# Kernel optimization log

Hardware: AMD Instinct MI355X
Metric: run time of the kernel (lower is better)

Reference implementation:

```python
import jax, jax.numpy as jnp
import numpy as np

B, S, D = 1, 2048, 4096
H = 32
Q_RANK, KV_RANK = 1536, 512
NOPE, ROPE, VD = 128, 64, 128
QD = NOPE + ROPE  # 192
EPS = 1e-6
THETA = 10000.0


def setup_inputs() -> dict:
    key = jax.random.key(0)
    ks = jax.random.split(key, 8)
    std = 0.02
    return {
        'hidden_states': jax.random.normal(ks[0], (B, S, D), jnp.float32),
        'Wq_a': jax.random.normal(ks[1], (D, Q_RANK), jnp.float32) * std,
        'q_a_ln_w': jnp.ones((Q_RANK,), jnp.float32),
        'Wq_b': jax.random.normal(ks[2], (Q_RANK, H * QD), jnp.float32) * std,
        'Wkv_a': jax.random.normal(ks[3], (D, KV_RANK + ROPE), jnp.float32) * std,
        'kv_a_ln_w': jnp.ones((KV_RANK,), jnp.float32),
        'Wkv_b': jax.random.normal(ks[4], (KV_RANK, H * (NOPE + VD)), jnp.float32) * std,
        'Wo': jax.random.normal(ks[5], (H * VD, D), jnp.float32) * std,
    }


def _rmsnorm(x, w):
    return x * jax.lax.rsqrt(jnp.mean(x * x, axis=-1, keepdims=True) + EPS) * w


def _rotate_half(x):
    h = x.shape[-1] // 2
    return jnp.concatenate([-x[..., h:], x[..., :h]], axis=-1)


def _apply_rope(x, cos, sin):
    # DeepSeek interleave permutation: view(..., d//2, 2).transpose -> [evens | odds]
    xp = jnp.concatenate([x[..., 0::2], x[..., 1::2]], axis=-1)
    return xp * cos + _rotate_half(xp) * sin


def _mla_forward(hidden_states, Wq_a, q_a_ln_w, Wq_b, Wkv_a, kv_a_ln_w, Wkv_b, Wo):
    b, s, _ = hidden_states.shape
    # low-rank query projection
    q = _rmsnorm(hidden_states @ Wq_a, q_a_ln_w) @ Wq_b          # [b,s,H*QD]
    q = q.reshape(b, s, H, QD).transpose(0, 2, 1, 3)             # [b,H,s,QD]
    q_nope, q_pe = q[..., :NOPE], q[..., NOPE:]
    # compressed kv + shared rope key
    ckv = hidden_states @ Wkv_a                                   # [b,s,KV_RANK+ROPE]
    compressed, k_pe = ckv[..., :KV_RANK], ckv[..., KV_RANK:]
    kv = _rmsnorm(compressed, kv_a_ln_w) @ Wkv_b                 # [b,s,H*(NOPE+VD)]
    kv = kv.reshape(b, s, H, NOPE + VD).transpose(0, 2, 1, 3)    # [b,H,s,NOPE+VD]
    k_nope, v = kv[..., :NOPE], kv[..., NOPE:]
    k_pe = k_pe[:, None, :, :]                                    # [b,1,s,ROPE]
    # rotary tables (cos/sin duplicated halves)
    inv_freq = 1.0 / (THETA ** (jnp.arange(0, ROPE, 2, dtype=jnp.float32) / ROPE))
    freqs = jnp.outer(jnp.arange(s, dtype=jnp.float32), inv_freq)  # [s,ROPE/2]
    emb = jnp.concatenate([freqs, freqs], axis=-1)                 # [s,ROPE]
    cos = jnp.cos(emb)[None, None].astype(hidden_states.dtype)
    sin = jnp.sin(emb)[None, None].astype(hidden_states.dtype)
    q_pe = _apply_rope(q_pe, cos, sin)
    k_pe = _apply_rope(k_pe, cos, sin)
    # assemble full q/k heads
    qf = jnp.concatenate([q_nope, q_pe], axis=-1)                 # [b,H,s,QD]
    kf = jnp.concatenate([k_nope, jnp.broadcast_to(k_pe, (b, H, s, ROPE))], axis=-1)
    scale = QD ** (-0.5)
    scores = jnp.einsum('bhqd,bhkd->bhqk', qf, kf) * scale        # [b,H,s,s]
    causal = jnp.tril(jnp.ones((s, s), dtype=bool))
    scores = jnp.where(causal, scores, jnp.finfo(scores.dtype).min)
    probs = jax.nn.softmax(scores, axis=-1)
    o = jnp.einsum('bhqk,bhkd->bhqd', probs, v)                   # [b,H,s,VD]
    o = o.transpose(0, 2, 1, 3).reshape(b, s, H * VD)
    return o @ Wo


def reference(hidden_states, Wq_a, q_a_ln_w, Wq_b, Wkv_a, kv_a_ln_w, Wkv_b, Wo):
    return _mla_forward(hidden_states, Wq_a, q_a_ln_w, Wq_b, Wkv_a, kv_a_ln_w, Wkv_b, Wo)
```

## Files before the change

kernel.cpp:

```cpp
#include <hip/hip_runtime.h>

typedef unsigned short u16;
using bf16x8 = __attribute__((ext_vector_type(8))) __bf16;
using f32x4  = __attribute__((ext_vector_type(4))) float;
using s16x8  = __attribute__((ext_vector_type(8))) short;
using s16x4  = __attribute__((ext_vector_type(4))) short;

#define AS1 __attribute__((address_space(1)))
#define AS3 __attribute__((address_space(3)))

__device__ __forceinline__ void gload16(const u16* g, u16* l) {
  __builtin_amdgcn_global_load_lds((AS1 void*)(size_t)g, (AS3 void*)l, 16, 0, 0);
}

__device__ __forceinline__ u16 f2bf(float f) {
  unsigned u = __float_as_uint(f);
  u += 0x7fffu + ((u >> 16) & 1u);
  return (u16)(u >> 16);
}
__device__ __forceinline__ float bf2f(u16 h) {
  return __uint_as_float(((unsigned)h) << 16);
}

__device__ __forceinline__ void transpose_tile(const float* __restrict__ W,
                                               u16* __restrict__ WT,
                                               int K, int N, int nb, int kb,
                                               u16 (*tile)[72]) {
  const int t = threadIdx.x;
  const int rr = t >> 3;
  const int cc = (t & 7) * 8;
#pragma unroll
  for (int pass = 0; pass < 2; ++pass) {
    const float* src = W + (size_t)(kb + pass * 32 + rr) * N + nb + cc;
    float4 a = *reinterpret_cast<const float4*>(src);
    float4 b = *reinterpret_cast<const float4*>(src + 4);
    u16* tr = &tile[pass * 32 + rr][cc];
    tr[0] = f2bf(a.x); tr[1] = f2bf(a.y); tr[2] = f2bf(a.z); tr[3] = f2bf(a.w);
    tr[4] = f2bf(b.x); tr[5] = f2bf(b.y); tr[6] = f2bf(b.z); tr[7] = f2bf(b.w);
  }
  __syncthreads();
#pragma unroll
  for (int pass = 0; pass < 2; ++pass) {
    s16x8 v;
#pragma unroll
    for (int j = 0; j < 8; ++j) v[j] = (short)tile[cc + j][pass * 32 + rr];
    *reinterpret_cast<s16x8*>(WT + (size_t)(nb + pass * 32 + rr) * K + kb + cc) = v;
  }
}

__global__ __launch_bounds__(256) void prep_merged_kernel(
    const float* __restrict__ hs, u16* __restrict__ hs_bf,
    const float* __restrict__ Wqa, const float* __restrict__ Wkva, u16* __restrict__ WabT,
    const float* __restrict__ Wqb, u16* __restrict__ WqbT,
    const float* __restrict__ Wkvb, u16* __restrict__ WkvbT,
    const float* __restrict__ Wo, u16* __restrict__ WoT,
    float* __restrict__ cost, float* __restrict__ sint) {
  __shared__ u16 tile[64][72];
  const int bid = blockIdx.x, t = threadIdx.x;
  if (bid < 8192) {
    int i = (bid * 256 + t) * 4;
    float4 v = *reinterpret_cast<const float4*>(hs + i);
    s16x4 o;
    o[0] = (short)f2bf(v.x); o[1] = (short)f2bf(v.y);
    o[2] = (short)f2bf(v.z); o[3] = (short)f2bf(v.w);
    *reinterpret_cast<s16x4*>(hs_bf + i) = o;
  } else if (bid < 9728) {
    int r = bid - 8192;
    transpose_tile(Wqa, WabT, 4096, 1536, (r % 24) * 64, (r / 24) * 64, tile);
  } else if (bid < 10304) {
    int r = bid - 9728;
    transpose_tile(Wkva, WabT + (size_t)1536 * 4096, 4096, 576, (r % 9) * 64, (r / 9) * 64, tile);
  } else if (bid < 12608) {
    int r = bid - 10304;
    transpose_tile(Wqb, WqbT, 1536, 6144, (r % 96) * 64, (r / 96) * 64, tile);
  } else if (bid < 13632) {
    int r = bid - 12608;
    transpose_tile(Wkvb, WkvbT, 512, 8192, (r % 128) * 64, (r / 128) * 64, tile);
  } else if (bid < 17728) {
    int r = bid - 13632;
    transpose_tile(Wo, WoT, 4096, 4096, (r % 64) * 64, (r / 64) * 64, tile);
  } else {
    int idx = (bid - 17728) * 256 + t;
    int pos = idx >> 5, j = idx & 31;
    float inv = __expf(-(float)j * (9.210340371976184f / 32.0f));
    float f = (float)pos * inv;
    cost[idx] = cosf(f);
    sint[idx] = sinf(f);
  }
}

__global__ __launch_bounds__(256) void norms_merged_kernel(const u16* __restrict__ fused,
                                                           const float* __restrict__ qln,
                                                           const float* __restrict__ kvln,
                                                           u16* __restrict__ qan,
                                                           u16* __restrict__ cn) {
  const int bid = blockIdx.x, t = threadIdx.x;
  const int row = bid & 2047;
  const bool is_q = bid < 2048;
  const int R = is_q ? 1536 : 512;
  const u16* xr = fused + (size_t)row * 2112 + (is_q ? 0 : 1536);
  const float* w = is_q ? qln : kvln;
  u16* yr = (is_q ? qan + (size_t)row * 1536 : cn + (size_t)row * 512);
  float ss = 0.f;
  for (int i = t; i < R; i += 256) { float f = bf2f(xr[i]); ss += f * f; }
#pragma unroll
  for (int m = 32; m >= 1; m >>= 1) ss += __shfl_xor(ss, m);
  __shared__ float red[4];
  if ((t & 63) == 0) red[t >> 6] = ss;
  __syncthreads();
  float tot = red[0] + red[1] + red[2] + red[3];
  float r = rsqrtf(tot / (float)R + 1e-6f);
  for (int i = t; i < R; i += 256) yr[i] = f2bf(bf2f(xr[i]) * r * w[i]);
}

__global__ __launch_bounds__(256) void builds_merged_kernel(const u16* __restrict__ q,
                                                            const u16* __restrict__ ckv,
                                                            const float* __restrict__ cost,
                                                            const float* __restrict__ sint,
                                                            u16* __restrict__ qf,
                                                            u16* __restrict__ kf) {
  const int bid = blockIdx.x, t = threadIdx.x;
  if (bid < 6144) {
    int o8 = (bid * 256 + t) * 8;
    const float scale = 0.07216878364870323f;
    int c = (o8 % 192) >> 3;
    int rest = o8 / 192;
    int s = rest & 2047, h = rest >> 11;
    const u16* qrow = q + ((size_t)s * 32 + h) * 192;
    s16x8 out;
    if (c < 16) {
      s16x8 v = *reinterpret_cast<const s16x8*>(qrow + c * 8);
#pragma unroll
      for (int j = 0; j < 8; ++j) out[j] = (short)f2bf(bf2f((u16)v[j]) * scale);
    } else {
      int j0 = c * 8 - 128;
      bool lo = j0 < 32;
      int jj0 = lo ? j0 : j0 - 32;
      s16x8 a = *reinterpret_cast<const s16x8*>(qrow + 128 + 2 * jj0);
      s16x8 b = *reinterpret_cast<const s16x8*>(qrow + 128 + 2 * jj0 + 8);
      float4 c0 = *reinterpret_cast<const float4*>(cost + s * 32 + jj0);
      float4 c1 = *reinterpret_cast<const float4*>(cost + s * 32 + jj0 + 4);
      float4 s0 = *reinterpret_cast<const float4*>(sint + s * 32 + jj0);
      float4 s1 = *reinterpret_cast<const float4*>(sint + s * 32 + jj0 + 4);
      float cs[8] = {c0.x, c0.y, c0.z, c0.w, c1.x, c1.y, c1.z, c1.w};
      float sn[8] = {s0.x, s0.y, s0.z, s0.w, s1.x, s1.y, s1.z, s1.w};
#pragma unroll
      for (int j = 0; j < 8; ++j) {
        float x0 = bf2f((u16)((j < 4) ? a[2 * j] : b[2 * j - 8]));
        float x1 = bf2f((u16)((j < 4) ? a[2 * j + 1] : b[2 * j - 7]));
        float v = lo ? (x0 * cs[j] - x1 * sn[j]) : (x1 * cs[j] + x0 * sn[j]);
        out[j] = (short)f2bf(v * scale);
      }
    }
    *reinterpret_cast<s16x8*>(qf + o8) = out;
  } else {
    int o8 = ((bid - 6144) * 256 + t) * 8;
    int j0 = o8 & 63;
    int rest = o8 >> 6;
    int s = rest & 2047, h = rest >> 11;
    bool lo = j0 < 32;
    int jj0 = lo ? j0 : j0 - 32;
    const u16* crow = ckv + (size_t)s * 2112 + 512;
    s16x8 a = *reinterpret_cast<const s16x8*>(crow + 2 * jj0);
    s16x8 b = *reinterpret_cast<const s16x8*>(crow + 2 * jj0 + 8);
    float4 c0 = *reinterpret_cast<const float4*>(cost + s * 32 + jj0);
    float4 c1 = *reinterpret_cast<const float4*>(cost + s * 32 + jj0 + 4);
    float4 s0 = *reinterpret_cast<const float4*>(sint + s * 32 + jj0);
    float4 s1 = *reinterpret_cast<const float4*>(sint + s * 32 + jj0 + 4);
    float cs[8] = {c0.x, c0.y, c0.z, c0.w, c1.x, c1.y, c1.z, c1.w};
    float sn[8] = {s0.x, s0.y, s0.z, s0.w, s1.x, s1.y, s1.z, s1.w};
    s16x8 out;
#pragma unroll
    for (int j = 0; j < 8; ++j) {
      float x0 = bf2f((u16)((j < 4) ? a[2 * j] : b[2 * j - 8]));
      float x1 = bf2f((u16)((j < 4) ? a[2 * j + 1] : b[2 * j - 7]));
      float v = lo ? (x0 * cs[j] - x1 * sn[j]) : (x1 * cs[j] + x0 * sn[j]);
      out[j] = (short)f2bf(v);
    }
    *reinterpret_cast<s16x8*>(kf + ((size_t)h * 2048 + s) * 192 + 128 + j0) = out;
  }
}

template <int EPI>
__device__ __forceinline__ void gemm_v3_body(const u16* __restrict__ A,
                                             const u16* __restrict__ BT,
                                             void* __restrict__ Cv,
                                             void* __restrict__ Cv2,
                                             int M, int N, int K,
                                             int bx, int by, u16* S) {
  const int t0 = threadIdx.x;
  const int lane = t0 & 63, wave = t0 >> 6;
  const int wr = wave >> 1, wc = wave & 1;
  const int row0 = by * 128, col0 = bx * 128;
  const int lrow = lane & 15, lkg = lane >> 4;

  const int lp = lane ^ ((lane >> 3) & 3);
  const int srow_off = lp >> 2;
  const int skel = (lp & 3) * 8;
  const int c0 = wave * 2, c1 = c0 + 1;
  const int arow_c0 = row0 + c0 * 16 + srow_off;
  const int arow_c1 = row0 + c1 * 16 + srow_off;
  int brow_c0 = col0 + c0 * 16 + srow_off; if (brow_c0 > N - 1) brow_c0 = N - 1;
  int brow_c1 = col0 + c1 * 16 + srow_off; if (brow_c1 > N - 1) brow_c1 = N - 1;

  int aoff[4], boff[4];
#pragma unroll
  for (int m = 0; m < 4; ++m) {
    int r = wr * 64 + m * 16 + lrow;
    int off = r * 32 + lkg * 8;
    aoff[m] = off ^ ((off >> 3) & 0x18);
    r = wc * 64 + m * 16 + lrow;
    off = r * 32 + lkg * 8;
    boff[m] = off ^ ((off >> 3) & 0x18);
  }

  const int NT = K >> 5;

#pragma unroll
  for (int pt = 0; pt < 3; ++pt) {
    u16* ab = &S[pt * 8192];
    const int kb = pt * 32 + skel;
    gload16(A  + (size_t)arow_c0 * K + kb, ab + c0 * 512);
    gload16(A  + (size_t)arow_c1 * K + kb, ab + c1 * 512);
    gload16(BT + (size_t)brow_c0 * K + kb, ab + 4096 + c0 * 512);
    gload16(BT + (size_t)brow_c1 * K + kb, ab + 4096 + c1 * 512);
  }

  f32x4 acc[4][4];
#pragma unroll
  for (int m = 0; m < 4; ++m)
#pragma unroll
    for (int n = 0; n < 4; ++n) acc[m][n] = 0.f;

  for (int t = 0; t < NT; ++t) {
    if (t + 2 < NT)      asm volatile("s_waitcnt vmcnt(8)" ::: "memory");
    else if (t + 1 < NT) asm volatile("s_waitcnt vmcnt(4)" ::: "memory");
    else                 asm volatile("s_waitcnt vmcnt(0)" ::: "memory");
    __builtin_amdgcn_s_barrier();
    __builtin_amdgcn_sched_barrier(0);

    const u16* ab = &S[(t & 3) * 8192];
    bf16x8 af[4], bb[4];
#pragma unroll
    for (int m = 0; m < 4; ++m)
      af[m] = *reinterpret_cast<const bf16x8*>(ab + aoff[m]);
#pragma unroll
    for (int n = 0; n < 4; ++n)
      bb[n] = *reinterpret_cast<const bf16x8*>(ab + 4096 + boff[n]);

    if (t + 3 < NT) {
      u16* sb = &S[((t + 3) & 3) * 8192];
      const int kb = (t + 3) * 32 + skel;
      gload16(A  + (size_t)arow_c0 * K + kb, sb + c0 * 512);
      gload16(A  + (size_t)arow_c1 * K + kb, sb + c1 * 512);
      gload16(BT + (size_t)brow_c0 * K + kb, sb + 4096 + c0 * 512);
      gload16(BT + (size_t)brow_c1 * K + kb, sb + 4096 + c1 * 512);
    }

    __builtin_amdgcn_s_setprio(1);
#pragma unroll
    for (int m = 0; m < 4; ++m)
#pragma unroll
      for (int n = 0; n < 4; ++n)
        acc[m][n] = __builtin_amdgcn_mfma_f32_16x16x32_bf16(af[m], bb[n], acc[m][n], 0, 0, 0);
    __builtin_amdgcn_s_setprio(0);
  }

#pragma unroll
  for (int m = 0; m < 4; ++m) {
#pragma unroll
    for (int n = 0; n < 4; ++n) {
      int col = col0 + wc * 64 + n * 16 + lrow;
      int row = row0 + wr * 64 + m * 16 + lkg * 4;
      if (EPI == 2) {
        int d = col & 255, hh = col >> 8;
        if (d < 128) {
          u16* dst = (u16*)Cv + ((size_t)hh * 2048 + row) * 192 + d;
#pragma unroll
          for (int i = 0; i < 4; ++i) dst[(size_t)i * 192] = f2bf(acc[m][n][i]);
        } else {
          s16x4 v;
#pragma unroll
          for (int i = 0; i < 4; ++i) v[i] = (short)f2bf(acc[m][n][i]);
          *reinterpret_cast<s16x4*>((u16*)Cv2 + ((size_t)hh * 128 + (d - 128)) * 2048 + row) = v;
        }
      } else if (col < N) {
#pragma unroll
        for (int i = 0; i < 4; ++i) {
          size_t idx = (size_t)(row + i) * N + col;
          if (EPI == 1) ((u16*)Cv)[idx] = f2bf(acc[m][n][i]);
          else          ((float*)Cv)[idx] = acc[m][n][i];
        }
      }
    }
  }
}

template <int EPI>
__global__ __launch_bounds__(256) void gemm_v3_kernel(const u16* __restrict__ A,
                                                      const u16* __restrict__ BT,
                                                      void* __restrict__ Cv,
                                                      void* __restrict__ Cv2,
                                                      int M, int N, int K) {
  __shared__ __align__(16) u16 S[4 * 8192];
  gemm_v3_body<EPI>(A, BT, Cv, Cv2, M, N, K, blockIdx.x, blockIdx.y, S);
}

__global__ __launch_bounds__(256) void gemm_qkv_kernel(const u16* __restrict__ qan,
                                                       const u16* __restrict__ WqbT,
                                                       u16* __restrict__ qout,
                                                       const u16* __restrict__ cn,
                                                       const u16* __restrict__ WkvbT,
                                                       u16* __restrict__ kfb,
                                                       u16* __restrict__ vTb) {
  __shared__ __align__(16) u16 S[4 * 8192];
  if (blockIdx.z == 0) {
    if (blockIdx.x >= 48) return;
    gemm_v3_body<1>(qan, WqbT, qout, nullptr, 2048, 6144, 1536, blockIdx.x, blockIdx.y, S);
  } else {
    gemm_v3_body<2>(cn, WkvbT, kfb, vTb, 2048, 8192, 512, blockIdx.x, blockIdx.y, S);
  }
}

__global__ __launch_bounds__(256) void mla_attn_kernel(const u16* __restrict__ qf,
                                                       const u16* __restrict__ kf,
                                                       const u16* __restrict__ vT,
                                                       u16* __restrict__ o) {
  const int h = blockIdx.x, pair = blockIdx.y;
  const int t = threadIdx.x, wave = t >> 6, lane = t & 63;
  const int lrow = lane & 15, lkg = lane >> 4;
  __shared__ __align__(16) u16 Kt[24 * 512];
  __shared__ __align__(16) u16 Vt[16 * 512];
  __shared__ __align__(16) u16 Pl[4][16][72];

  const u16* ksrc0 = kf + ((size_t)h * 2048 + wave * 16 + lrow) * 192 + lkg * 8;
  const u16* vsrc0 = vT + ((size_t)h * 128 + wave * 32 + lrow) * 2048 + lkg * 8;

  for (int qq = 0; qq < 2; ++qq) {
    const int qb = qq ? (31 - pair) : pair;
    const int qbase = qb * 64 + wave * 16;

    bf16x8 qfr[6];
    const u16* qrow_ptr = qf + ((size_t)h * 2048 + qbase + lrow) * 192;
#pragma unroll
    for (int kk = 0; kk < 6; ++kk)
      qfr[kk] = *reinterpret_cast<const bf16x8*>(qrow_ptr + kk * 32 + lkg * 8);

    f32x4 acc_o[8];
#pragma unroll
    for (int f = 0; f < 8; ++f) acc_o[f] = 0.f;
    float m_run[4], l_par[4];
#pragma unroll
    for (int i = 0; i < 4; ++i) { m_run[i] = -1e30f; l_par[i] = 0.f; }

    const int kv_end = qb * 64 + 64;
    for (int kt = 0; kt < kv_end; kt += 64) {
      {
        const u16* ks = ksrc0 + (size_t)kt * 192;
#pragma unroll
        for (int kk = 0; kk < 6; ++kk)
          gload16(ks + kk * 32, &Kt[(wave * 6 + kk) * 512]);
#pragma unroll
        for (int j = 0; j < 4; ++j) {
          int fo = (j >> 1), ck = j & 1;
          gload16(vsrc0 + (size_t)fo * 16 * 2048 + kt + ck * 32,
                  &Vt[((wave * 2 + fo) * 2 + ck) * 512]);
        }
      }
      __syncthreads();

      f32x4 sv[4];
#pragma unroll
      for (int cg = 0; cg < 4; ++cg) sv[cg] = 0.f;
#pragma unroll
      for (int cg = 0; cg < 4; ++cg)
#pragma unroll
        for (int kk = 0; kk < 6; ++kk) {
          bf16x8 kfr = *reinterpret_cast<const bf16x8*>(&Kt[(cg * 6 + kk) * 512 + lane * 8]);
          sv[cg] = __builtin_amdgcn_mfma_f32_16x16x32_bf16(qfr[kk], kfr, sv[cg], 0, 0, 0);
        }

      const int qrow_b = qbase + lkg * 4;
      if (kt + 64 >= kv_end) {
#pragma unroll
        for (int cg = 0; cg < 4; ++cg) {
          int kvcol = kt + cg * 16 + lrow;
#pragma unroll
          for (int i = 0; i < 4; ++i)
            if (kvcol > qrow_b + i) sv[cg][i] = -__builtin_inff();
        }
      }
      float tmax[4];
#pragma unroll
      for (int i = 0; i < 4; ++i)
        tmax[i] = fmaxf(fmaxf(sv[0][i], sv[1][i]), fmaxf(sv[2][i], sv[3][i]));
#pragma unroll
      for (int m = 8; m >= 1; m >>= 1)
#pragma unroll
        for (int i = 0; i < 4; ++i) tmax[i] = fmaxf(tmax[i], __shfl_xor(tmax[i], m));
      int need = 0;
#pragma unroll
      for (int i = 0; i < 4; ++i) need |= (tmax[i] > m_run[i] + 8.f) ? 1 : 0;
      if (__any(need)) {
#pragma unroll
        for (int i = 0; i < 4; ++i) {
          float mnew = fmaxf(m_run[i], tmax[i]);
          float alpha = __expf(m_run[i] - mnew);
          m_run[i] = mnew;
          l_par[i] *= alpha;
#pragma unroll
          for (int f = 0; f < 8; ++f) acc_o[f][i] *= alpha;
        }
      }
#pragma unroll
      for (int i = 0; i < 4; ++i) {
#pragma unroll
        for (int cg = 0; cg < 4; ++cg) sv[cg][i] = __expf(sv[cg][i] - m_run[i]);
        l_par[i] += (sv[0][i] + sv[1][i]) + (sv[2][i] + sv[3][i]);
      }
#pragma unroll
      for (int cg = 0; cg < 4; ++cg)
#pragma unroll
        for (int i = 0; i < 4; ++i)
          Pl[wave][lkg * 4 + i][cg * 16 + lrow] = f2bf(sv[cg][i]);
#pragma unroll
      for (int ck = 0; ck < 2; ++ck) {
        bf16x8 pf = *reinterpret_cast<const bf16x8*>(&Pl[wave][lrow][ck * 32 + lkg * 8]);
#pragma unroll
        for (int f = 0; f < 8; ++f) {
          bf16x8 vfr = *reinterpret_cast<const bf16x8*>(&Vt[(f * 2 + ck) * 512 + lane * 8]);
          acc_o[f] = __builtin_amdgcn_mfma_f32_16x16x32_bf16(pf, vfr, acc_o[f], 0, 0, 0);
        }
      }
      __syncthreads();
    }
#pragma unroll
    for (int i = 0; i < 4; ++i)
#pragma unroll
      for (int m = 8; m >= 1; m >>= 1) l_par[i] += __shfl_xor(l_par[i], m);
#pragma unroll
    for (int f = 0; f < 8; ++f)
#pragma unroll
      for (int i = 0; i < 4; ++i) {
        int row = qbase + lkg * 4 + i;
        int col = h * 128 + f * 16 + lrow;
        o[(size_t)row * 4096 + col] = f2bf(acc_o[f][i] / l_par[i]);
      }
  }
}

extern "C" void kernel_launch(void* const* d_in, const int* in_sizes, int n_in,
                              void* d_out, int out_size, void* d_ws, size_t ws_size,
                              hipStream_t stream) {
  (void)in_sizes; (void)n_in; (void)out_size; (void)ws_size;
  const float* hs   = (const float*)d_in[0];
  const float* Wqa  = (const float*)d_in[1];
  const float* qln  = (const float*)d_in[2];
  const float* Wqb  = (const float*)d_in[3];
  const float* Wkva = (const float*)d_in[4];
  const float* kvln = (const float*)d_in[5];
  const float* Wkvb = (const float*)d_in[6];
  const float* Wo   = (const float*)d_in[7];
  float* out = (float*)d_out;

  char* p = (char*)d_ws;
  size_t off = 0;
  auto carve = [&](size_t bytes) {
    char* r = p + off;
    off += (bytes + 255) & ~(size_t)255;
    return r;
  };
  u16* hs_bf = (u16*)carve((size_t)2048 * 4096 * 2);
  u16* WabT  = (u16*)carve((size_t)2112 * 4096 * 2);
  u16* WqbT  = (u16*)carve((size_t)6144 * 1536 * 2);
  u16* WkvbT = (u16*)carve((size_t)8192 * 512 * 2);
  u16* WoT   = (u16*)carve((size_t)4096 * 4096 * 2);
  u16* fused = (u16*)carve((size_t)2048 * 2112 * 2);
  u16* qan   = (u16*)carve((size_t)2048 * 1536 * 2);
  u16* q     = (u16*)carve((size_t)2048 * 6144 * 2);
  u16* cn    = (u16*)carve((size_t)2048 * 512 * 2);
  u16* qfb   = (u16*)carve((size_t)32 * 2048 * 192 * 2);
  u16* kfb   = (u16*)carve((size_t)32 * 2048 * 192 * 2);
  u16* vTb   = (u16*)carve((size_t)32 * 128 * 2048 * 2);
  u16* ob    = (u16*)carve((size_t)2048 * 4096 * 2);
  float* cost = (float*)carve((size_t)65536 * 4);
  float* sint = (float*)carve((size_t)65536 * 4);

  prep_merged_kernel<<<17984, 256, 0, stream>>>(hs, hs_bf, Wqa, Wkva, WabT,
                                                Wqb, WqbT, Wkvb, WkvbT, Wo, WoT,
                                                cost, sint);

  gemm_v3_kernel<1><<<dim3(17, 16), 256, 0, stream>>>(hs_bf, WabT, fused, nullptr, 2048, 2112, 4096);

  norms_merged_kernel<<<4096, 256, 0, stream>>>(fused, qln, kvln, qan, cn);

  gemm_qkv_kernel<<<dim3(64, 16, 2), 256, 0, stream>>>(qan, WqbT, q, cn, WkvbT, kfb, vTb);

  builds_merged_kernel<<<8192, 256, 0, stream>>>(q, fused + 1536, cost, sint, qfb, kfb);

  mla_attn_kernel<<<dim3(32, 16), 256, 0, stream>>>(qfb, kfb, vTb, ob);

  gemm_v3_kernel<0><<<dim3(32, 16), 256, 0, stream>>>(ob, WoT, out, nullptr, 2048, 4096, 4096);
}
```

Measured before the change: 404.8 us.

## Double-buffer K/V tiles with 32-wide KV steps and per-wave causal skip

The attention kernel now processes KV in 32-column tiles held in double-buffered LDS. The next tile is prefetched with async global_load_lds before the current one is computed, and explicit vmcnt waits and barriers replace __syncthreads. Waves whose query rows lie entirely before the current KV tile skip compute, which trims causal waste. The aim is to hide global load latency and reduce masked work, at the cost of twice as many barriers per KV column and hand-tuned waitcnt sequencing that could be fragile.

```diff
diff --git a/kernel.cpp b/kernel.cpp
--- a/kernel.cpp
+++ b/kernel.cpp
@@ -329,12 +329,26 @@
   const int h = blockIdx.x, pair = blockIdx.y;
   const int t = threadIdx.x, wave = t >> 6, lane = t & 63;
   const int lrow = lane & 15, lkg = lane >> 4;
-  __shared__ __align__(16) u16 Kt[24 * 512];
-  __shared__ __align__(16) u16 Vt[16 * 512];
-  __shared__ __align__(16) u16 Pl[4][16][72];
-
-  const u16* ksrc0 = kf + ((size_t)h * 2048 + wave * 16 + lrow) * 192 + lkg * 8;
-  const u16* vsrc0 = vT + ((size_t)h * 128 + wave * 32 + lrow) * 2048 + lkg * 8;
+  __shared__ __align__(16) u16 Kt[2][12 * 512];
+  __shared__ __align__(16) u16 Vt[2][8 * 512];
+  __shared__ __align__(16) u16 Pl[4][16][36];
+
+  const u16* ksrc[3]; u16 *kdst0[3], *kdst1[3];
+#pragma unroll
+  for (int i = 0; i < 3; ++i) {
+    int c = wave * 3 + i, cg = c / 6, kk = c - cg * 6;
+    ksrc[i] = kf + ((size_t)h * 2048 + cg * 16 + lrow) * 192 + kk * 32 + lkg * 8;
+    kdst0[i] = &Kt[0][c * 512];
+    kdst1[i] = &Kt[1][c * 512];
+  }
+  const u16* vsrc[2]; u16 *vdst0[2], *vdst1[2];
+#pragma unroll
+  for (int j = 0; j < 2; ++j) {
+    int f = wave * 2 + j;
+    vsrc[j] = vT + ((size_t)h * 128 + f * 16 + lrow) * 2048 + lkg * 8;
+    vdst0[j] = &Vt[0][f * 512];
+    vdst1[j] = &Vt[1][f * 512];
+  }
 
   for (int qq = 0; qq < 2; ++qq) {
     const int qb = qq ? (31 - pair) : pair;
@@ -353,86 +367,93 @@
 #pragma unroll
     for (int i = 0; i < 4; ++i) { m_run[i] = -1e30f; l_par[i] = 0.f; }
 
-    const int kv_end = qb * 64 + 64;
-    for (int kt = 0; kt < kv_end; kt += 64) {
-      {
-        const u16* ks = ksrc0 + (size_t)kt * 192;
-#pragma unroll
-        for (int kk = 0; kk < 6; ++kk)
-          gload16(ks + kk * 32, &Kt[(wave * 6 + kk) * 512]);
-#pragma unroll
-        for (int j = 0; j < 4; ++j) {
-          int fo = (j >> 1), ck = j & 1;
-          gload16(vsrc0 + (size_t)fo * 16 * 2048 + kt + ck * 32,
-                  &Vt[((wave * 2 + fo) * 2 + ck) * 512]);
+    const int nt = 2 * qb + 2;
+
+#pragma unroll
+    for (int i = 0; i < 3; ++i) gload16(ksrc[i], kdst0[i]);
+#pragma unroll
+    for (int j = 0; j < 2; ++j) gload16(vsrc[j], vdst0[j]);
+
+    for (int it = 0; it < nt; ++it) {
+      const int kt = it * 32;
+      if (it + 1 < nt) {
+        const int nb = (it + 1) & 1;
+        const size_t kadv = (size_t)(it + 1) * 32 * 192;
+        const size_t vadv = (size_t)(it + 1) * 32;
+#pragma unroll
+        for (int i = 0; i < 3; ++i) gload16(ksrc[i] + kadv, nb ? kdst1[i] : kdst0[i]);
+#pragma unroll
+        for (int j = 0; j < 2; ++j) gload16(vsrc[j] + vadv, nb ? vdst1[j] : vdst0[j]);
+        asm volatile("s_waitcnt vmcnt(5)" ::: "memory");
+      } else {
+        asm volatile("s_waitcnt vmcnt(0)" ::: "memory");
+      }
+      __builtin_amdgcn_s_barrier();
+      __builtin_amdgcn_sched_barrier(0);
+
+      const u16* Kb = &Kt[it & 1][0];
+      const u16* Vb = &Vt[it & 1][0];
+      if (kt <= qbase + 15) {
+        f32x4 sv[2];
+        sv[0] = 0.f; sv[1] = 0.f;
+#pragma unroll
+        for (int cg = 0; cg < 2; ++cg)
+#pragma unroll
+          for (int kk = 0; kk < 6; ++kk) {
+            bf16x8 kfr = *reinterpret_cast<const bf16x8*>(&Kb[(cg * 6 + kk) * 512 + lane * 8]);
+            sv[cg] = __builtin_amdgcn_mfma_f32_16x16x32_bf16(qfr[kk], kfr, sv[cg], 0, 0, 0);
+          }
+        const int qrow_b = qbase + lkg * 4;
+        if (kt + 31 > qbase) {
+#pragma unroll
+          for (int cg = 0; cg < 2; ++cg) {
+            int kvcol = kt + cg * 16 + lrow;
+#pragma unroll
+            for (int i = 0; i < 4; ++i)
+              if (kvcol > qrow_b + i) sv[cg][i] = -__builtin_inff();
+          }
         }
-      }
-      __syncthreads();
-
-      f32x4 sv[4];
-#pragma unroll
-      for (int cg = 0; cg < 4; ++cg) sv[cg] = 0.f;
-#pragma unroll
-      for (int cg = 0; cg < 4; ++cg)
-#pragma unroll
-        for (int kk = 0; kk < 6; ++kk) {
-          bf16x8 kfr = *reinterpret_cast<const bf16x8*>(&Kt[(cg * 6 + kk) * 512 + lane * 8]);
-          sv[cg] = __builtin_amdgcn_mfma_f32_16x16x32_bf16(qfr[kk], kfr, sv[cg], 0, 0, 0);
+        float tmax[4];
+#pragma unroll
+        for (int i = 0; i < 4; ++i) tmax[i] = fmaxf(sv[0][i], sv[1][i]);
+#pragma unroll
+        for (int m = 8; m >= 1; m >>= 1)
+#pragma unroll
+          for (int i = 0; i < 4; ++i) tmax[i] = fmaxf(tmax[i], __shfl_xor(tmax[i], m));
+        int need = 0;
+#pragma unroll
+        for (int i = 0; i < 4; ++i) need |= (tmax[i] > m_run[i] + 8.f) ? 1 : 0;
+        if (__any(need)) {
+#pragma unroll
+          for (int i = 0; i < 4; ++i) {
+            float mnew = fmaxf(m_run[i], tmax[i]);
+            float alpha = __expf(m_run[i] - mnew);
+            m_run[i] = mnew;
+            l_par[i] *= alpha;
+#pragma unroll
+            for (int f = 0; f < 8; ++f) acc_o[f][i] *= alpha;
+          }
         }
-
-      const int qrow_b = qbase + lkg * 4;
-      if (kt + 64 >= kv_end) {
-#pragma unroll
-        for (int cg = 0; cg < 4; ++cg) {
-          int kvcol = kt + cg * 16 + lrow;
+#pragma unroll
+        for (int i = 0; i < 4; ++i) {
+          sv[0][i] = __expf(sv[0][i] - m_run[i]);
+          sv[1][i] = __expf(sv[1][i] - m_run[i]);
+          l_par[i] += sv[0][i] + sv[1][i];
+        }
+#pragma unroll
+        for (int cg = 0; cg < 2; ++cg)
 #pragma unroll
           for (int i = 0; i < 4; ++i)
-            if (kvcol > qrow_b + i) sv[cg][i] = -__builtin_inff();
-        }
-      }
-      float tmax[4];
-#pragma unroll
-      for (int i = 0; i < 4; ++i)
-        tmax[i] = fmaxf(fmaxf(sv[0][i], sv[1][i]), fmaxf(sv[2][i], sv[3][i]));
-#pragma unroll
-      for (int m = 8; m >= 1; m >>= 1)
-#pragma unroll
-        for (int i = 0; i < 4; ++i) tmax[i] = fmaxf(tmax[i], __shfl_xor(tmax[i], m));
-      int need = 0;
-#pragma unroll
-      for (int i = 0; i < 4; ++i) need |= (tmax[i] > m_run[i] + 8.f) ? 1 : 0;
-      if (__any(need)) {
-#pragma unroll
-        for (int i = 0; i < 4; ++i) {
-          float mnew = fmaxf(m_run[i], tmax[i]);
-          float alpha = __expf(m_run[i] - mnew);
-          m_run[i] = mnew;
-          l_par[i] *= alpha;
-#pragma unroll
-          for (int f = 0; f < 8; ++f) acc_o[f][i] *= alpha;
-        }
-      }
-#pragma unroll
-      for (int i = 0; i < 4; ++i) {
-#pragma unroll
-        for (int cg = 0; cg < 4; ++cg) sv[cg][i] = __expf(sv[cg][i] - m_run[i]);
-        l_par[i] += (sv[0][i] + sv[1][i]) + (sv[2][i] + sv[3][i]);
-      }
-#pragma unroll
-      for (int cg = 0; cg < 4; ++cg)
-#pragma unroll
-        for (int i = 0; i < 4; ++i)
-          Pl[wave][lkg * 4 + i][cg * 16 + lrow] = f2bf(sv[cg][i]);
-#pragma unroll
-      for (int ck = 0; ck < 2; ++ck) {
-        bf16x8 pf = *reinterpret_cast<const bf16x8*>(&Pl[wave][lrow][ck * 32 + lkg * 8]);
+            Pl[wave][lkg * 4 + i][cg * 16 + lrow] = f2bf(sv[cg][i]);
+        bf16x8 pf = *reinterpret_cast<const bf16x8*>(&Pl[wave][lrow][lkg * 8]);
 #pragma unroll
         for (int f = 0; f < 8; ++f) {
-          bf16x8 vfr = *reinterpret_cast<const bf16x8*>(&Vt[(f * 2 + ck) * 512 + lane * 8]);
+          bf16x8 vfr = *reinterpret_cast<const bf16x8*>(&Vb[f * 512 + lane * 8]);
           acc_o[f] = __builtin_amdgcn_mfma_f32_16x16x32_bf16(pf, vfr, acc_o[f], 0, 0, 0);
         }
       }
-      __syncthreads();
+      __builtin_amdgcn_sched_barrier(0);
+      __builtin_amdgcn_s_barrier();
     }
 #pragma unroll
     for (int i = 0; i < 4; ++i)
```

New measurement: 403.1 us. No clear change (-0.4%).
